# Performance work log

Measured on AMD Instinct MI355X. Metric: run time of the kernel, lower is better.

The kernel has to match this reference:

```python
import jax, jax.numpy as jnp
import numpy as np

GRID_SIZE, SPLINE_ORDER = 5, 3  # efficient-kan KANLinear defaults
NUM_BASES = GRID_SIZE + SPLINE_ORDER


def b_splines(x, grid):
    # x: (N, in_dim), grid: (in_dim, GRID_SIZE + 2*SPLINE_ORDER + 1)
    xe = x[..., None]
    bases = ((xe >= grid[:, :-1]) & (xe < grid[:, 1:])).astype(x.dtype)
    for k in range(1, SPLINE_ORDER + 1):  # Cox-de Boor recursion (static, 3 iters)
        left = (xe - grid[:, : -(k + 1)]) / (grid[:, k:-1] - grid[:, : -(k + 1)])
        right = (grid[:, k + 1:] - xe) / (grid[:, k + 1:] - grid[:, 1:-k])
        bases = left * bases[..., :-1] + right * bases[..., 1:]
    return bases  # (N, in_dim, NUM_BASES)


def kan_linear(x, grid, base_w, spline_w, scaler):
    # base branch: SiLU(x) @ W_base^T ; spline branch: B-spline basis @ scaled spline weights
    n = x.shape[0]
    out_dim = base_w.shape[0]
    base = jax.nn.silu(x) @ base_w.T
    bs = b_splines(x, grid).reshape(n, -1)                    # (N, in*NUM_BASES)
    sw = (spline_w * scaler[..., None]).reshape(out_dim, -1)  # (out, in*NUM_BASES)
    return base + bs @ sw.T


def setup_inputs() -> dict:
    key = jax.random.key(0)
    N, E, F, H, C, L = 50000, 500000, 128, 128, 40, 3
    ks = jax.random.split(key, 8)
    x = jax.random.normal(ks[0], (N, F), dtype=jnp.float32)
    edge_index = jax.random.randint(ks[1], (2, E), 0, N)
    # KAN grid (registered buffer in efficient-kan): uniform over [-1,1] extended by spline_order
    h_step = 2.0 / GRID_SIZE
    pts = np.arange(-SPLINE_ORDER, GRID_SIZE + SPLINE_ORDER + 1) * h_step - 1.0
    grid_mp = jnp.asarray(np.tile(pts, (F, 1)), dtype=jnp.float32)
    D = F + L * H  # skip-concat dim into output KANLinear
    grid_out = jnp.asarray(np.tile(pts, (D, 1)), dtype=jnp.float32)
    s = 0.1
    conv_base_w = jax.random.normal(ks[2], (L, H, F), dtype=jnp.float32) * s
    conv_spline_w = jax.random.normal(ks[3], (L, H, F, NUM_BASES), dtype=jnp.float32) * s
    conv_scaler = jnp.ones((L, H, F), dtype=jnp.float32)
    conv_bias = jnp.zeros((L, H), dtype=jnp.float32)
    bn_gamma = jnp.ones((L, H), dtype=jnp.float32)
    bn_beta = jnp.zeros((L, H), dtype=jnp.float32)
    out_base_w = jax.random.normal(ks[4], (C, D), dtype=jnp.float32) * s
    out_spline_w = jax.random.normal(ks[5], (C, D, NUM_BASES), dtype=jnp.float32) * s
    out_scaler = jnp.ones((C, D), dtype=jnp.float32)
    return dict(x=x, edge_index=edge_index, grid_mp=grid_mp, conv_base_w=conv_base_w,
                conv_spline_w=conv_spline_w, conv_scaler=conv_scaler, conv_bias=conv_bias,
                bn_gamma=bn_gamma, bn_beta=bn_beta, grid_out=grid_out,
                out_base_w=out_base_w, out_spline_w=out_spline_w, out_scaler=out_scaler)


def reference(x, edge_index, grid_mp, conv_base_w, conv_spline_w, conv_scaler, conv_bias,
              bn_gamma, bn_beta, grid_out, out_base_w, out_spline_w, out_scaler):
    N = x.shape[0]
    L = conv_base_w.shape[0]
    # GCN normalization with self-loops (computed once; identical each layer)
    loop = jnp.arange(N)
    src = jnp.concatenate([edge_index[0], loop])
    dst = jnp.concatenate([edge_index[1], loop])
    deg = jax.ops.segment_sum(jnp.ones_like(src, dtype=x.dtype), dst, num_segments=N)
    dinv = jnp.where(deg > 0, jax.lax.rsqrt(jnp.maximum(deg, 1.0)), 0.0)
    norm = dinv[src] * dinv[dst]  # (E+N,)
    feats = [x]
    for i in range(L):  # static layer loop
        h = kan_linear(x, grid_mp, conv_base_w[i], conv_spline_w[i], conv_scaler[i])
        # symmetric-normalized sparse aggregation (gather on src, scatter-add on dst)
        h = jax.ops.segment_sum(h[src] * norm[:, None], dst, num_segments=N) + conv_bias[i]
        # BatchNorm1d (training mode: biased batch statistics over nodes)
        mu = h.mean(axis=0)
        var = h.var(axis=0)
        x = (h - mu) * jax.lax.rsqrt(var + 1e-5) * bn_gamma[i] + bn_beta[i]
        feats.append(x)  # dropout p=0.0 is identity
    xc = jnp.concatenate(feats, axis=1)  # skip-concat: (N, F + L*H)
    logits = kan_linear(xc, grid_out, out_base_w, out_spline_w, out_scaler)
    return jax.nn.log_softmax(logits, axis=1)
```

## Files before the change

kernel.cpp:

```cpp
#include <hip/hip_runtime.h>
#include <hip/hip_bf16.h>
#include <math.h>

#define F_IN   128
#define HID    128
#define NLAYER 3
#define NCLS   40
#define DCAT   512
#define OOUT   64

typedef short s16x8 __attribute__((ext_vector_type(8)));
typedef unsigned short u16x8 __attribute__((ext_vector_type(8)));
typedef unsigned short u16x4 __attribute__((ext_vector_type(4)));
typedef float f32x4 __attribute__((ext_vector_type(4)));
typedef unsigned long long u64x2 __attribute__((ext_vector_type(2)));


static __device__ __forceinline__ float silu_f(float x) {
    return x / (1.f + __expf(-x));
}

static __device__ __forceinline__ unsigned short f2bf_rn(float f) {
    union { __hip_bfloat16 h; unsigned short u; } cv;
    cv.h = __float2bfloat16(f);
    return cv.u;
}

static __device__ __forceinline__ float bf2f(unsigned short u) {
    return __uint_as_float((unsigned)u << 16);
}

static __device__ __forceinline__ void lds_barrier() {
    asm volatile("s_waitcnt lgkmcnt(0)" ::: "memory");
    __builtin_amdgcn_s_barrier();
}


__global__ __launch_bounds__(256) void deg_count_kernel(const int* __restrict__ dst, int E, int* deg) {
    for (int i = blockIdx.x * blockDim.x + threadIdx.x; i < E; i += gridDim.x * blockDim.x)
        atomicAdd(&deg[dst[i]], 1);
}

__global__ __launch_bounds__(256) void scan_reduce_kernel(const int* __restrict__ deg, int* __restrict__ bsum, int N) {
    __shared__ int sh[256];
    int t = threadIdx.x;
    int e = blockIdx.x * 256 + t;
    sh[t] = (e < N) ? deg[e] + 1 : 0;
    __syncthreads();
#pragma unroll
    for (int off = 128; off > 0; off >>= 1) {
        if (t < off) sh[t] += sh[t + off];
        __syncthreads();
    }
    if (t == 0) bsum[blockIdx.x] = sh[0];
}

__global__ __launch_bounds__(256) void scan_top_kernel(const int* __restrict__ bsum, int* __restrict__ bbase, int nsb) {
    __shared__ int sh[256];
    int t = threadIdx.x;
    int chunk = (nsb + 255) >> 8;
    int begin = t * chunk;
    int end = begin + chunk; if (end > nsb) end = nsb;
    int s = 0;
    for (int i = begin; i < end; ++i) s += bsum[i];
    sh[t] = s;
    __syncthreads();
#pragma unroll
    for (int off = 1; off < 256; off <<= 1) {
        int v = 0;
        if (t >= off) v = sh[t - off];
        __syncthreads();
        if (t >= off) sh[t] += v;
        __syncthreads();
    }
    int run = (t == 0) ? 0 : sh[t - 1];
    for (int i = begin; i < end; ++i) {
        bbase[i] = run;
        run += bsum[i];
    }
}

__global__ __launch_bounds__(256) void scan_write_kernel(const int* __restrict__ deg,
                                                         const int* __restrict__ bbase,
                                                         int* __restrict__ offs, int* __restrict__ cursor,
                                                         float* __restrict__ dinv, int N) {
    __shared__ int sh[256];
    int t = threadIdx.x;
    int e = blockIdx.x * 256 + t;
    int d = (e < N) ? deg[e] + 1 : 0;
    sh[t] = d;
    __syncthreads();
#pragma unroll
    for (int off = 1; off < 256; off <<= 1) {
        int v = 0;
        if (t >= off) v = sh[t - off];
        __syncthreads();
        if (t >= off) sh[t] += v;
        __syncthreads();
    }
    int incl = sh[t] + bbase[blockIdx.x];
    int excl = incl - d;
    if (e < N) {
        offs[e] = excl;
        cursor[e] = excl;
        dinv[e] = rsqrtf((float)d);
        if (e == N - 1) offs[N] = incl;
    }
}

__global__ __launch_bounds__(256) void fill_kernel(const int* __restrict__ src, const int* __restrict__ dst,
                                                   int E, int N, int* cursor, int* __restrict__ csr) {
    int total = E + N;
    for (int i = blockIdx.x * blockDim.x + threadIdx.x; i < total; i += gridDim.x * blockDim.x) {
        if (i < E) {
            int d = dst[i];
            int p = atomicAdd(&cursor[d], 1);
            csr[p] = src[i];
        } else {
            int n = i - E;
            int p = atomicAdd(&cursor[n], 1);
            csr[p] = n;
        }
    }
}

#define TC_PACK (NLAYER * 9 * 4 * 8 * 64 * 8)
#define TO_PACK (36 * 4 * 4 * 64 * 8)
__global__ __launch_bounds__(256) void pack_all_kernel(const float* __restrict__ cbw,
                                                       const float* __restrict__ csw,
                                                       const float* __restrict__ csc,
                                                       const float* __restrict__ obw,
                                                       const float* __restrict__ osw,
                                                       const float* __restrict__ osc,
                                                       unsigned short* __restrict__ wpkc,
                                                       unsigned short* __restrict__ wpko,
                                                       float* __restrict__ scA, float* __restrict__ shA) {
    int gid0 = blockIdx.x * blockDim.x + threadIdx.x;
    if (gid0 < 128) { scA[gid0] = 1.f; shA[gid0] = 0.f; }
    int total = TC_PACK + TO_PACK;
    for (int idx = gid0; idx < total; idx += gridDim.x * blockDim.x) {
        if (idx < TC_PACK) {
            int e    = idx & 7;
            int lane = (idx >> 3) & 63;
            int cf   = (idx >> 9) & 7;
            int kk   = (idx >> 12) & 3;
            int cc   = (idx >> 14) % 9;
            int l    = idx / (9 << 14);
            int o = cf * 16 + (lane & 15);
            int k = kk * 32 + ((lane >> 4) << 3) + e;
            float v;
            if (cc == 8) {
                v = cbw[(l * 128 + o) * 128 + k];
            } else {
                int f = cc * 16 + (k >> 3);
                int j = k & 7;
                int base = (l * 128 + o) * 128 + f;
                v = csw[base * 8 + j] * csc[base];
            }
            wpkc[idx] = f2bf_rn(v);
        } else {
            int ix = idx - TC_PACK;
            int e    = ix & 7;
            int lane = (ix >> 3) & 63;
            int cf   = (ix >> 9) & 3;
            int kk   = (ix >> 11) & 3;
            int gcc  = ix >> 13;
            int g = gcc / 9, cc = gcc % 9;
            int o = cf * 16 + (lane & 15);
            int k = kk * 32 + ((lane >> 4) << 3) + e;
            float v = 0.f;
            if (o < NCLS) {
                if (cc == 8) {
                    int f = g * 128 + k;
                    v = obw[o * DCAT + f];
                } else {
                    int f = g * 128 + cc * 16 + (k >> 3);
                    int j = k & 7;
                    int base = o * DCAT + f;
                    v = osw[base * 8 + j] * osc[base];
                }
            }
            wpko[ix] = f2bf_rn(v);
        }
    }
}

template<bool CONV, bool INIT>
__global__ __launch_bounds__(256, 2) void kan_fused_kernel(
    const float* __restrict__ xin, int xstride, int in_off,
    const float* __restrict__ scA, const float* __restrict__ shA,
    const unsigned short* __restrict__ wconv,
    const unsigned short* __restrict__ wout,
    unsigned short* __restrict__ htmp,
    const float* __restrict__ dinv,
    float* __restrict__ out_acc, int N) {

    __shared__ __align__(16) char lds_phi0[16384];
    __shared__ __align__(16) char lds_phi1[16384];

    const int tid = threadIdx.x;
    const int lane = tid & 63;
    const int wave = tid >> 6;
    const int l15 = lane & 15, lg = lane >> 4;
    const int nblk = blockIdx.x * 64;

    const float g0 = -1.f - 3.f * 0.4f;
    const float invh = 1.f / 0.4f;

    const int fg = tid & 3;
    const int n0 = tid >> 2;

    f32x4 accc[4][2];
    f32x4 acco[4];
    if (CONV) {
#pragma unroll
        for (int r = 0; r < 4; ++r)
#pragma unroll
            for (int c = 0; c < 2; ++c) accc[r][c] = (f32x4)0.f;
    }
#pragma unroll
    for (int r = 0; r < 4; ++r) acco[r] = (f32x4)0.f;

    float4 xqb[2], scb[2], shb[2];
    auto ldx = [&](int cc, int slot) {
        int f0 = in_off + cc * 16 + fg * 4;
        scb[slot] = *(const float4*)(scA + f0);
        shb[slot] = *(const float4*)(shA + f0);
        int gn = nblk + n0;
        xqb[slot] = (gn < N) ? *(const float4*)(xin + (size_t)gn * xstride + f0)
                             : (float4){0.f, 0.f, 0.f, 0.f};
    };

    s16x8 wc_reg[4][2];
    s16x8 wo_reg[4];
    auto loadW = [&](int cc) {
        if (CONV) {
            const unsigned short* wcb = wconv + (size_t)cc * 16384;
#pragma unroll
            for (int kk = 0; kk < 4; ++kk)
#pragma unroll
                for (int c = 0; c < 2; ++c) {
                    int cf = wave * 2 + c;
                    wc_reg[kk][c] = *(const s16x8*)(wcb + (((size_t)kk * 8 + cf) * 64 + lane) * 8);
                }
        }
        const unsigned short* wob = wout + (size_t)cc * 8192;
#pragma unroll
        for (int kk = 0; kk < 4; ++kk)
            wo_reg[kk] = *(const s16x8*)(wob + (((size_t)kk * 4 + wave) * 64 + lane) * 8);
    };

    u16x4 sreg[8];

    u64x2 pcur[4];
    auto phi_compute = [&](int ccc, int slot) {
        float xi[4] = {xqb[slot].x, xqb[slot].y, xqb[slot].z, xqb[slot].w};
        float scr[4] = {scb[slot].x, scb[slot].y, scb[slot].z, scb[slot].w};
        float shr[4] = {shb[slot].x, shb[slot].y, shb[slot].z, shb[slot].w};
        u16x4 sv;
#pragma unroll
        for (int fl = 0; fl < 4; ++fl) {
            float y = fmaf(xi[fl], scr[fl], shr[fl]);
            sv[fl] = f2bf_rn(silu_f(y));
            float t = (y - g0) * invh;
            float cfl = floorf(t);
            int c = (int)cfl;
            c = c < -20 ? -20 : (c > 20 ? 20 : c);
            float u = t - cfl;
            float um = 1.f - u;
            float u2 = u * u;
            float um2 = um * um;
            float w0 = um2 * um * (1.f / 6.f);
            float w3 = u2 * u * (1.f / 6.f);
            float w1 = fmaf(fmaf(0.5f, u, -1.f), u2, 2.f / 3.f);
            float w2 = fmaf(fmaf(-0.5f, u, 0.5f), u2, fmaf(0.5f, u, 1.f / 6.f));
            unsigned long long W = (unsigned long long)f2bf_rn(w0)
                                 | ((unsigned long long)f2bf_rn(w1) << 16)
                                 | ((unsigned long long)f2bf_rn(w2) << 32)
                                 | ((unsigned long long)f2bf_rn(w3) << 48);
            int pos = (c - 3) * 16;
            unsigned long long lo = (pos >= 0) ? (W << (pos & 63)) : (W >> ((-pos) & 63));
            lo = (pos >= 64 || pos <= -64) ? 0ull : lo;
            int ph = pos - 64;
            unsigned long long hi = (ph >= 0) ? (W << (ph & 63)) : (W >> ((-ph) & 63));
            hi = (ph >= 64 || ph <= -64) ? 0ull : hi;
            u64x2 v; v.x = lo; v.y = hi;
            pcur[fl] = v;
        }
        sreg[ccc] = sv;
    };

    auto write_phi = [&](char* buf) {
        int swz = (n0 & 7) << 4;
#pragma unroll
        for (int i = 0; i < 4; ++i) {
            int byte = n0 * 256 + ((fg * 64 + i * 16) ^ swz);
            *(u64x2*)(buf + byte) = pcur[i];
        }
    };

    auto write_silu = [&](char* buf) {
        int swz = (n0 & 7) << 4;
#pragma unroll
        for (int ccc = 0; ccc < 8; ++ccc) {
            int byte = n0 * 256 + (((ccc * 16 + fg * 4) * 2) ^ swz);
            *(u16x4*)(buf + byte) = sreg[ccc];
        }
    };

    auto mfma_phase = [&](const char* buf) {
#pragma unroll
        for (int kk = 0; kk < 4; ++kk) {
            const int kb = kk * 64 + lg * 16;
            s16x8 af[4];
#pragma unroll
            for (int r = 0; r < 4; ++r) {
                int n = r * 16 + l15;
                af[r] = *(const s16x8*)(buf + n * 256 + (kb ^ ((n & 7) << 4)));
            }
            if (CONV) {
#pragma unroll
                for (int c = 0; c < 2; ++c)
#pragma unroll
                    for (int r = 0; r < 4; ++r)
                        accc[r][c] = __builtin_amdgcn_mfma_f32_16x16x32_bf16(af[r], wc_reg[kk][c], accc[r][c], 0, 0, 0);
            }
#pragma unroll
            for (int r = 0; r < 4; ++r)
                acco[r] = __builtin_amdgcn_mfma_f32_16x16x32_bf16(af[r], wo_reg[kk], acco[r], 0, 0, 0);
        }
    };

    ldx(0, 0);
    phi_compute(0, 0);
    ldx(1, 1);
    loadW(0);
    write_phi(lds_phi0);
    __syncthreads();

#pragma unroll
    for (int cc = 0; cc < 9; ++cc) {
        char* cur = (cc & 1) ? lds_phi1 : lds_phi0;
        char* nxt = (cc & 1) ? lds_phi0 : lds_phi1;
        if (cc < 7) ldx(cc + 2, cc & 1);
        mfma_phase(cur);
        if (cc < 8) loadW(cc + 1);
        if (cc < 7) {
            phi_compute(cc + 1, (cc + 1) & 1);
            write_phi(nxt);
        }
        if (cc == 7) write_silu(nxt);
        if (cc < 8) lds_barrier();
    }

#pragma unroll
    for (int r = 0; r < 4; ++r) {
        int nb = nblk + r * 16 + lg * 4;
        if (CONV) {
#pragma unroll
            for (int c = 0; c < 2; ++c) {
                int o = wave * 32 + c * 16 + l15;
#pragma unroll
                for (int q = 0; q < 4; ++q) {
                    int n = nb + q;
                    if (n < N) htmp[(size_t)n * HID + o] = f2bf_rn(accc[r][c][q] * dinv[n]);
                }
            }
        }
        {
            int o = wave * 16 + l15;
            if (o < NCLS) {
#pragma unroll
                for (int q = 0; q < 4; ++q) {
                    int n = nb + q;
                    if (n < N) {
                        size_t a = (size_t)n * OOUT + o;
                        float v = acco[r][q];
                        if (!INIT) v += out_acc[a];
                        out_acc[a] = v;
                    }
                }
            }
        }
    }
}

__global__ __launch_bounds__(256) void agg_kernel(const unsigned short* __restrict__ h,
                                                  const float* __restrict__ dinv,
                                                  const int* __restrict__ offs,
                                                  const int* __restrict__ csr,
                                                  const float* __restrict__ bias,
                                                  float* __restrict__ xc, int out_off, int N) {
    int n = blockIdx.x * 4 + (threadIdx.x >> 6);
    if (n >= N) return;
    int lane = threadIdx.x & 63;
    int eg = lane >> 4;
    int cg = lane & 15;
    int s = offs[n], e = offs[n + 1];

    float acc[4][8];
#pragma unroll
    for (int a = 0; a < 4; ++a)
#pragma unroll
        for (int k = 0; k < 8; ++k) acc[a][k] = 0.f;

    for (int base = s; base < e; base += 64) {
        int cnt = e - base; if (cnt > 64) cnt = 64;
        int ci = base + lane;
        int cv = (ci < e) ? csr[ci] : 0;

#pragma unroll
        for (int j = 0; j < 4; ++j) {
            int ei = j * 4 + eg;
            int v = __shfl(cv, ei);
            if (ei < cnt) {
                u16x8 hv = *(const u16x8*)(h + (size_t)v * HID + cg * 8);
#pragma unroll
                for (int k = 0; k < 8; ++k) acc[j][k] += bf2f(hv[k]);
            }
        }
        int nj = (cnt + 3) >> 2;
        for (int j = 4; j < nj; ++j) {
            int ei = j * 4 + eg;
            int v = __shfl(cv, ei);
            if (ei < cnt) {
                u16x8 hv = *(const u16x8*)(h + (size_t)v * HID + cg * 8);
#pragma unroll
                for (int k = 0; k < 8; ++k) acc[j & 3][k] += bf2f(hv[k]);
            }
        }
    }

    float tot[8];
#pragma unroll
    for (int k = 0; k < 8; ++k)
        tot[k] = (acc[0][k] + acc[1][k]) + (acc[2][k] + acc[3][k]);
#pragma unroll
    for (int k = 0; k < 8; ++k) {
        tot[k] += __shfl_xor(tot[k], 16);
        tot[k] += __shfl_xor(tot[k], 32);
    }
    if (eg == 0) {
        float dn = dinv[n];
        float4 b0 = *(const float4*)(bias + cg * 8);
        float4 b1 = *(const float4*)(bias + cg * 8 + 4);
        float4 o0 = {fmaf(tot[0], dn, b0.x), fmaf(tot[1], dn, b0.y),
                     fmaf(tot[2], dn, b0.z), fmaf(tot[3], dn, b0.w)};
        float4 o1 = {fmaf(tot[4], dn, b1.x), fmaf(tot[5], dn, b1.y),
                     fmaf(tot[6], dn, b1.z), fmaf(tot[7], dn, b1.w)};
        float* dst = xc + (size_t)n * DCAT + out_off + cg * 8;
        *(float4*)dst = o0;
        *(float4*)(dst + 4) = o1;
    }
}

__global__ __launch_bounds__(128) void bn_stats_kernel(const float* __restrict__ xc, int off, int N,
                                                       float* __restrict__ bnsum, float* __restrict__ bnsq,
                                                       const float* __restrict__ gamma,
                                                       const float* __restrict__ beta,
                                                       float* scA, float* shA, int seg_off, float invN,
                                                       int* __restrict__ counter) {
    __shared__ int last;
    int f = threadIdx.x;
    float s = 0.f, q = 0.f;
    for (int n = blockIdx.x; n < N; n += gridDim.x) {
        float v = xc[(size_t)n * DCAT + off + f];
        s += v;
        q += v * v;
    }
    atomicAdd(&bnsum[f], s);
    atomicAdd(&bnsq[f], q);
    __threadfence();
    __syncthreads();
    if (f == 0) {
        int t = atomicAdd(counter, 1);
        last = (t == (int)gridDim.x - 1);
    }
    __syncthreads();
    if (last) {
        float mu = bnsum[f] * invN;
        float var = bnsq[f] * invN - mu * mu;
        float rs = rsqrtf(var + 1e-5f);
        float sc = gamma[f] * rs;
        scA[seg_off + f] = sc;
        shA[seg_off + f] = fmaf(-mu, sc, beta[f]);
        if (f == 0) *counter = 0;
    }
}

__global__ __launch_bounds__(256) void logsoftmax_kernel(const float* __restrict__ oacc,
                                                         float* __restrict__ out, int N) {
    for (int n = blockIdx.x * blockDim.x + threadIdx.x; n < N; n += gridDim.x * blockDim.x) {
        const float* row = oacc + (size_t)n * OOUT;
        float m = -1e30f;
#pragma unroll
        for (int j = 0; j < NCLS; ++j) m = fmaxf(m, row[j]);
        float s = 0.f;
#pragma unroll
        for (int j = 0; j < NCLS; ++j) s += __expf(row[j] - m);
        float lse = m + __logf(s);
        float* orow = out + (size_t)n * NCLS;
#pragma unroll
        for (int j = 0; j < NCLS; ++j) orow[j] = row[j] - lse;
    }
}


extern "C" void kernel_launch(void* const* d_in, const int* in_sizes, int n_in,
                              void* d_out, int out_size, void* d_ws, size_t ws_size,
                              hipStream_t stream) {
    const float* x            = (const float*)d_in[0];
    const int*   eidx         = (const int*)d_in[1];
    const float* conv_base_w  = (const float*)d_in[3];
    const float* conv_spline_w= (const float*)d_in[4];
    const float* conv_scaler  = (const float*)d_in[5];
    const float* conv_bias    = (const float*)d_in[6];
    const float* bn_gamma     = (const float*)d_in[7];
    const float* bn_beta      = (const float*)d_in[8];
    const float* out_base_w   = (const float*)d_in[10];
    const float* out_spline_w = (const float*)d_in[11];
    const float* out_scaler   = (const float*)d_in[12];
    float* out = (float*)d_out;

    int N = in_sizes[0] / F_IN;
    int E = in_sizes[1] / 2;
    const int* esrc = eidx;
    const int* edst = eidx + E;

    int blocks = (N + 63) / 64;
    int npad = blocks * 64;
    int nsb = (N + 255) / 256;

    char* p = (char*)d_ws;
    auto carve = [&](size_t bytes) {
        char* r = p;
        p += (bytes + 255) & ~(size_t)255;
        return r;
    };
    float* xc   = (float*)carve((size_t)N * DCAT * 4);
    unsigned short* htmp = (unsigned short*)carve((size_t)npad * HID * 2);
    float* oacc = (float*)carve((size_t)npad * OOUT * 4);
    float* dinv = (float*)carve((size_t)N * 4);
    float* bn   = (float*)carve((size_t)NLAYER * 2 * HID * 4 + 256);
    int* counter = (int*)(bn + NLAYER * 2 * HID);
    float* scA  = (float*)carve((size_t)DCAT * 4);
    float* shA  = (float*)carve((size_t)DCAT * 4);
    unsigned short* wpkc = (unsigned short*)carve((size_t)NLAYER * 9 * 128 * 128 * 2);
    unsigned short* wpko = (unsigned short*)carve((size_t)36 * 64 * 128 * 2);
    int* deg    = (int*)carve((size_t)N * 4);
    int* offs   = (int*)carve((size_t)(N + 1) * 4);
    int* cursor = (int*)carve((size_t)(N + 1) * 4);
    int* bsum   = (int*)carve((size_t)nsb * 4);
    int* bbase  = (int*)carve((size_t)nsb * 4);
    int* csr    = (int*)carve((size_t)(E + N) * 4);

    hipMemsetAsync(bn, 0, NLAYER * 2 * HID * 4 + 256, stream);
    hipMemsetAsync(deg, 0, (size_t)N * 4, stream);

    deg_count_kernel<<<1024, 256, 0, stream>>>(edst, E, deg);
    scan_reduce_kernel<<<nsb, 256, 0, stream>>>(deg, bsum, N);
    scan_top_kernel<<<1, 256, 0, stream>>>(bsum, bbase, nsb);
    scan_write_kernel<<<nsb, 256, 0, stream>>>(deg, bbase, offs, cursor, dinv, N);
    fill_kernel<<<1024, 256, 0, stream>>>(esrc, edst, E, N, cursor, csr);

    pack_all_kernel<<<1024, 256, 0, stream>>>(conv_base_w, conv_spline_w, conv_scaler,
                                              out_base_w, out_spline_w, out_scaler,
                                              wpkc, wpko, scA, shA);

    float invN = 1.f / (float)N;
    for (int l = 0; l < NLAYER; ++l) {
        int in_off = l * HID;
        int out_off = (l + 1) * HID;
        const unsigned short* wl = wpkc + (size_t)l * 9 * 16384;
        const unsigned short* wo = wpko + (size_t)l * 9 * 8192;
        if (l == 0)
            kan_fused_kernel<true, true><<<blocks, 256, 0, stream>>>(
                x, F_IN, 0, scA, shA, wl, wo, htmp, dinv, oacc, N);
        else
            kan_fused_kernel<true, false><<<blocks, 256, 0, stream>>>(
                xc, DCAT, in_off, scA, shA, wl, wo, htmp, dinv, oacc, N);
        agg_kernel<<<(N + 3) / 4, 256, 0, stream>>>(htmp, dinv, offs, csr, conv_bias + l * HID, xc, out_off, N);
        float* bnsum = bn + l * 2 * HID;
        float* bnsq  = bnsum + HID;
        bn_stats_kernel<<<256, 128, 0, stream>>>(xc, out_off, N, bnsum, bnsq,
                                                 bn_gamma + l * HID, bn_beta + l * HID,
                                                 scA, shA, out_off, invN, counter);
    }

    kan_fused_kernel<false, false><<<blocks, 256, 0, stream>>>(
        xc, DCAT, 384, scA, shA, nullptr, wpko + (size_t)3 * 9 * 8192, htmp, dinv, oacc, N);

    logsoftmax_kernel<<<(N + 255) / 256, 256, 0, stream>>>(oacc, out, N);
}
```

Before: 518.9 us.

## Split fused KAN kernel work across 8 waves instead of 4

Doubles the block size of the fused KAN kernel to 512 threads. Each wave now owns one 16-column slice of the conv output instead of two, and only the first three waves compute the 40-class output projection. Each thread now handles 2 features in the spline/SiLU stage instead of 4. The intent is more latency hiding and less register pressure per thread, at the cost of idle waves on the output MFMAs and more threads contending at barriers.

```diff
diff --git a/kernel.cpp b/kernel.cpp
--- a/kernel.cpp
+++ b/kernel.cpp
@@ -12,6 +12,7 @@
 typedef short s16x8 __attribute__((ext_vector_type(8)));
 typedef unsigned short u16x8 __attribute__((ext_vector_type(8)));
 typedef unsigned short u16x4 __attribute__((ext_vector_type(4)));
+typedef unsigned short u16x2 __attribute__((ext_vector_type(2)));
 typedef float f32x4 __attribute__((ext_vector_type(4)));
 typedef unsigned long long u64x2 __attribute__((ext_vector_type(2)));
 
@@ -186,7 +187,7 @@
 }
 
 template<bool CONV, bool INIT>
-__global__ __launch_bounds__(256, 2) void kan_fused_kernel(
+__global__ __launch_bounds__(512, 2) void kan_fused_kernel(
     const float* __restrict__ xin, int xstride, int in_off,
     const float* __restrict__ scA, const float* __restrict__ shA,
     const unsigned short* __restrict__ wconv,
@@ -207,59 +208,57 @@
     const float g0 = -1.f - 3.f * 0.4f;
     const float invh = 1.f / 0.4f;
 
-    const int fg = tid & 3;
-    const int n0 = tid >> 2;
-
-    f32x4 accc[4][2];
+    const int fg2 = tid & 7;
+    const int n0 = tid >> 3;
+
+    const bool has_out = (wave < 3);
+
+    f32x4 accc[4];
     f32x4 acco[4];
     if (CONV) {
 #pragma unroll
-        for (int r = 0; r < 4; ++r)
-#pragma unroll
-            for (int c = 0; c < 2; ++c) accc[r][c] = (f32x4)0.f;
+        for (int r = 0; r < 4; ++r) accc[r] = (f32x4)0.f;
     }
 #pragma unroll
     for (int r = 0; r < 4; ++r) acco[r] = (f32x4)0.f;
 
-    float4 xqb[2], scb[2], shb[2];
+    float2 xqb[2], scb[2], shb[2];
     auto ldx = [&](int cc, int slot) {
-        int f0 = in_off + cc * 16 + fg * 4;
-        scb[slot] = *(const float4*)(scA + f0);
-        shb[slot] = *(const float4*)(shA + f0);
+        int f0 = in_off + cc * 16 + fg2 * 2;
+        scb[slot] = *(const float2*)(scA + f0);
+        shb[slot] = *(const float2*)(shA + f0);
         int gn = nblk + n0;
-        xqb[slot] = (gn < N) ? *(const float4*)(xin + (size_t)gn * xstride + f0)
-                             : (float4){0.f, 0.f, 0.f, 0.f};
-    };
-
-    s16x8 wc_reg[4][2];
+        xqb[slot] = (gn < N) ? *(const float2*)(xin + (size_t)gn * xstride + f0)
+                             : (float2){0.f, 0.f};
+    };
+
+    s16x8 wc_reg[4];
     s16x8 wo_reg[4];
     auto loadW = [&](int cc) {
         if (CONV) {
             const unsigned short* wcb = wconv + (size_t)cc * 16384;
 #pragma unroll
             for (int kk = 0; kk < 4; ++kk)
-#pragma unroll
-                for (int c = 0; c < 2; ++c) {
-                    int cf = wave * 2 + c;
-                    wc_reg[kk][c] = *(const s16x8*)(wcb + (((size_t)kk * 8 + cf) * 64 + lane) * 8);
-                }
-        }
-        const unsigned short* wob = wout + (size_t)cc * 8192;
-#pragma unroll
-        for (int kk = 0; kk < 4; ++kk)
-            wo_reg[kk] = *(const s16x8*)(wob + (((size_t)kk * 4 + wave) * 64 + lane) * 8);
-    };
-
-    u16x4 sreg[8];
-
-    u64x2 pcur[4];
+                wc_reg[kk] = *(const s16x8*)(wcb + (((size_t)kk * 8 + wave) * 64 + lane) * 8);
+        }
+        if (has_out) {
+            const unsigned short* wob = wout + (size_t)cc * 8192;
+#pragma unroll
+            for (int kk = 0; kk < 4; ++kk)
+                wo_reg[kk] = *(const s16x8*)(wob + (((size_t)kk * 4 + wave) * 64 + lane) * 8);
+        }
+    };
+
+    u16x2 sreg[8];
+
+    u64x2 pcur[2];
     auto phi_compute = [&](int ccc, int slot) {
-        float xi[4] = {xqb[slot].x, xqb[slot].y, xqb[slot].z, xqb[slot].w};
-        float scr[4] = {scb[slot].x, scb[slot].y, scb[slot].z, scb[slot].w};
-        float shr[4] = {shb[slot].x, shb[slot].y, shb[slot].z, shb[slot].w};
-        u16x4 sv;
-#pragma unroll
-        for (int fl = 0; fl < 4; ++fl) {
+        float xi[2] = {xqb[slot].x, xqb[slot].y};
+        float scr[2] = {scb[slot].x, scb[slot].y};
+        float shr[2] = {shb[slot].x, shb[slot].y};
+        u16x2 sv;
+#pragma unroll
+        for (int fl = 0; fl < 2; ++fl) {
             float y = fmaf(xi[fl], scr[fl], shr[fl]);
             sv[fl] = f2bf_rn(silu_f(y));
             float t = (y - g0) * invh;
@@ -293,8 +292,8 @@
     auto write_phi = [&](char* buf) {
         int swz = (n0 & 7) << 4;
 #pragma unroll
-        for (int i = 0; i < 4; ++i) {
-            int byte = n0 * 256 + ((fg * 64 + i * 16) ^ swz);
+        for (int i = 0; i < 2; ++i) {
+            int byte = n0 * 256 + ((fg2 * 32 + i * 16) ^ swz);
             *(u64x2*)(buf + byte) = pcur[i];
         }
     };
@@ -303,8 +302,8 @@
         int swz = (n0 & 7) << 4;
 #pragma unroll
         for (int ccc = 0; ccc < 8; ++ccc) {
-            int byte = n0 * 256 + (((ccc * 16 + fg * 4) * 2) ^ swz);
-            *(u16x4*)(buf + byte) = sreg[ccc];
+            int byte = n0 * 256 + (((ccc * 16 + fg2 * 2) * 2) ^ swz);
+            *(u16x2*)(buf + byte) = sreg[ccc];
         }
     };
 
@@ -320,14 +319,14 @@
             }
             if (CONV) {
 #pragma unroll
-                for (int c = 0; c < 2; ++c)
-#pragma unroll
-                    for (int r = 0; r < 4; ++r)
-                        accc[r][c] = __builtin_amdgcn_mfma_f32_16x16x32_bf16(af[r], wc_reg[kk][c], accc[r][c], 0, 0, 0);
-            }
-#pragma unroll
-            for (int r = 0; r < 4; ++r)
-                acco[r] = __builtin_amdgcn_mfma_f32_16x16x32_bf16(af[r], wo_reg[kk], acco[r], 0, 0, 0);
+                for (int r = 0; r < 4; ++r)
+                    accc[r] = __builtin_amdgcn_mfma_f32_16x16x32_bf16(af[r], wc_reg[kk], accc[r], 0, 0, 0);
+            }
+            if (has_out) {
+#pragma unroll
+                for (int r = 0; r < 4; ++r)
+                    acco[r] = __builtin_amdgcn_mfma_f32_16x16x32_bf16(af[r], wo_reg[kk], acco[r], 0, 0, 0);
+            }
         }
     };
 
@@ -357,17 +356,14 @@
     for (int r = 0; r < 4; ++r) {
         int nb = nblk + r * 16 + lg * 4;
         if (CONV) {
-#pragma unroll
-            for (int c = 0; c < 2; ++c) {
-                int o = wave * 32 + c * 16 + l15;
-#pragma unroll
-                for (int q = 0; q < 4; ++q) {
-                    int n = nb + q;
-                    if (n < N) htmp[(size_t)n * HID + o] = f2bf_rn(accc[r][c][q] * dinv[n]);
-                }
-            }
-        }
-        {
+            int o = wave * 16 + l15;
+#pragma unroll
+            for (int q = 0; q < 4; ++q) {
+                int n = nb + q;
+                if (n < N) htmp[(size_t)n * HID + o] = f2bf_rn(accc[r][q] * dinv[n]);
+            }
+        }
+        if (has_out) {
             int o = wave * 16 + l15;
             if (o < NCLS) {
 #pragma unroll
@@ -574,10 +570,10 @@
         const unsigned short* wl = wpkc + (size_t)l * 9 * 16384;
         const unsigned short* wo = wpko + (size_t)l * 9 * 8192;
         if (l == 0)
-            kan_fused_kernel<true, true><<<blocks, 256, 0, stream>>>(
+            kan_fused_kernel<true, true><<<blocks, 512, 0, stream>>>(
                 x, F_IN, 0, scA, shA, wl, wo, htmp, dinv, oacc, N);
         else
-            kan_fused_kernel<true, false><<<blocks, 256, 0, stream>>>(
+            kan_fused_kernel<true, false><<<blocks, 512, 0, stream>>>(
                 xc, DCAT, in_off, scA, shA, wl, wo, htmp, dinv, oacc, N);
         agg_kernel<<<(N + 3) / 4, 256, 0, stream>>>(htmp, dinv, offs, csr, conv_bias + l * HID, xc, out_off, N);
         float* bnsum = bn + l * 2 * HID;
@@ -587,7 +583,7 @@
                                                  scA, shA, out_off, invN, counter);
     }
 
-    kan_fused_kernel<false, false><<<blocks, 256, 0, stream>>>(
+    kan_fused_kernel<false, false><<<blocks, 512, 0, stream>>>(
         xc, DCAT, 384, scA, shA, nullptr, wpko + (size_t)3 * 9 * 8192, htmp, dinv, oacc, N);
 
     logsoftmax_kernel<<<(N + 255) / 256, 256, 0, stream>>>(oacc, out, N);
```

Measured after the change: 551.7 us. 1.06x slower.
